# Optimization experiments

Measured on AMD Instinct MI355X. Metric: run time of the kernel, lower is better.

The kernel has to match this reference:

```python
import jax, jax.numpy as jnp
import numpy as np

N = 50000      # nodes
E = 800000     # edges (avg degree 16)
IN = 128       # in_dim == hidden_dim*num_heads so residuals fire
D = 32         # hidden_dim (per-head)
H = 4          # num_heads
OUT = 64       # out_dim (final layer has 1 head)
NEG_SLOPE = 0.2
LN_EPS = 1e-5


def setup_inputs() -> dict:
    key = jax.random.key(0)
    ks = jax.random.split(key, 16)
    rn = lambda k, s: jax.random.normal(k, s, jnp.float32) * 0.05
    return {
        "features": jax.random.normal(ks[0], (N, IN), jnp.float32),
        "edge_weight": jax.random.uniform(ks[1], (E,), jnp.float32),
        "src": jax.random.randint(ks[2], (E,), 0, N),
        "dst": jax.random.randint(ks[3], (E,), 0, N),
        "W0": rn(ks[4], (IN, H * D)), "al0": rn(ks[5], (H, D)), "ar0": rn(ks[6], (H, D)), "lam0": jnp.float32(1.0),
        "W1": rn(ks[7], (H * D, H * D)), "al1": rn(ks[8], (H, D)), "ar1": rn(ks[9], (H, D)), "lam1": jnp.float32(1.0),
        "W2": rn(ks[10], (H * D, OUT)), "al2": rn(ks[11], (1, OUT)), "ar2": rn(ks[12], (1, OUT)), "lam2": jnp.float32(1.0),
        "g0": jnp.ones((H * D,), jnp.float32), "b0": jnp.zeros((H * D,), jnp.float32),
        "g1": jnp.ones((H * D,), jnp.float32), "b1": jnp.zeros((H * D,), jnp.float32),
    }


def _gat_layer(h, W, al, ar, lam, src, dst, ew):
    n = h.shape[0]
    heads, d = al.shape
    ft = (h @ W).reshape(n, heads, d)                      # [N,H,D]
    el = jnp.sum(ft * al[None], axis=-1)                   # [N,H]
    er = jnp.sum(ft * ar[None], axis=-1)                   # [N,H]
    e = el[src] + er[dst] + lam * ew[:, None]              # [E,H] u_add_v + weight bias
    e = jax.nn.leaky_relu(e, NEG_SLOPE)
    # edge softmax over incoming edges of each dst node
    m = jax.ops.segment_max(e, dst, num_segments=n)        # [N,H]
    ex = jnp.exp(e - m[dst])
    s = jax.ops.segment_sum(ex, dst, num_segments=n)       # [N,H]
    a = ex / s[dst]                                        # [E,H]
    # u_mul_e + sum aggregation
    msg = ft[src] * a[:, :, None]                          # [E,H,D]
    return jax.ops.segment_sum(msg, dst, num_segments=n)   # [N,H,D]


def _layer_norm(x, g, b):
    mu = jnp.mean(x, axis=-1, keepdims=True)
    var = jnp.mean((x - mu) ** 2, axis=-1, keepdims=True)
    return (x - mu) * jax.lax.rsqrt(var + LN_EPS) * g + b


def _forward(features, edge_weight, src, dst,
             W0, al0, ar0, lam0, W1, al1, ar1, lam1, W2, al2, ar2, lam2,
             g0, b0, g1, b1):
    n = features.shape[0]
    h = features
    # layer 0
    h1 = _gat_layer(h, W0, al0, ar0, lam0, src, dst, edge_weight)
    h1 = jax.nn.elu(h1).reshape(n, -1)
    h1 = _layer_norm(h1, g0, b0)
    if h1.shape == h.shape:
        h1 = h1 + h
    # layer 1
    h2 = _gat_layer(h1, W1, al1, ar1, lam1, src, dst, edge_weight)
    h2 = jax.nn.elu(h2).reshape(n, -1)
    h2 = _layer_norm(h2, g1, b1)
    h2 = h2 + h1
    # layer 2 (single head, no activation)
    out = _gat_layer(h2, W2, al2, ar2, lam2, src, dst, edge_weight).reshape(n, -1)
    return out


def reference(features, edge_weight, src, dst,
              W0, al0, ar0, lam0, W1, al1, ar1, lam1, W2, al2, ar2, lam2,
              g0, b0, g1, b1):
    # eval mode: dropout off and _add_noise is identity, so noisy == clean
    h_clean = _forward(features, edge_weight, src, dst,
                       W0, al0, ar0, lam0, W1, al1, ar1, lam1, W2, al2, ar2, lam2,
                       g0, b0, g1, b1)
    return (h_clean, h_clean)
```

## Files before the change

kernel.cpp:

```cpp
#include <hip/hip_runtime.h>

#define NEG_SLOPE 0.2f
#define LN_EPS 1e-5f

typedef __attribute__((ext_vector_type(8))) short bf16x8;
typedef __attribute__((ext_vector_type(4))) float f32x4;

__device__ inline unsigned short f2bf(float f) {
    unsigned u = __float_as_uint(f);
    unsigned r = u + 0x7FFFu + ((u >> 16) & 1u);
    return (unsigned short)(r >> 16);
}

__device__ inline void unpack8(uint4 u, float* f) {
    f[0] = __uint_as_float(u.x << 16);
    f[1] = __uint_as_float(u.x & 0xFFFF0000u);
    f[2] = __uint_as_float(u.y << 16);
    f[3] = __uint_as_float(u.y & 0xFFFF0000u);
    f[4] = __uint_as_float(u.z << 16);
    f[5] = __uint_as_float(u.z & 0xFFFF0000u);
    f[6] = __uint_as_float(u.w << 16);
    f[7] = __uint_as_float(u.w & 0xFFFF0000u);
}


__global__ void prep_kernel(const int* __restrict__ dst, int* __restrict__ counts,
                            int* __restrict__ rank, int E, int RB,
                            const float* __restrict__ W0, const float* __restrict__ W1,
                            const float* __restrict__ W2, unsigned short* __restrict__ Wt0,
                            unsigned short* __restrict__ Wt1,
                            unsigned short* __restrict__ Wt2) {
    int bid = blockIdx.x;
    if (bid < RB) {
        int i = bid * 256 + threadIdx.x;
        if (i < E) rank[i] = atomicAdd(&counts[dst[i] * 16], 1);
    } else {
        int row = (bid - RB) * 2 + (threadIdx.x >> 7);
        int k = threadIdx.x & 127;
        if (row < 128) {
            Wt0[row * 128 + k] = f2bf(W0[k * 128 + row]);
        } else if (row < 256) {
            int c = row - 128;
            Wt1[c * 128 + k] = f2bf(W1[k * 128 + c]);
        } else {
            int c = row - 256;
            Wt2[c * 128 + k] = f2bf(W2[k * 64 + c]);
        }
    }
}

__global__ __launch_bounds__(256) void scan1_kernel(const int* __restrict__ counts,
                                                    int* __restrict__ bsum, int n) {
    __shared__ int lds[256];
    int t = threadIdx.x;
    int i = blockIdx.x * 256 + t;
    lds[t] = (i < n) ? counts[i * 16] : 0;
    __syncthreads();
    for (int off = 128; off > 0; off >>= 1) {
        int v = (t < off) ? lds[t + off] : 0;
        __syncthreads();
        if (t < off) lds[t] += v;
        __syncthreads();
    }
    if (t == 0) bsum[blockIdx.x] = lds[0];
}

__global__ __launch_bounds__(256) void scan3_kernel(const int* __restrict__ counts,
                                                    const int* __restrict__ bsum,
                                                    int* __restrict__ rowptr, int n, int E,
                                                    int nscan) {
    __shared__ int lds[256];
    int t = threadIdx.x;
    lds[t] = (t < nscan) ? bsum[t] : 0;
    __syncthreads();
    for (int off = 1; off < 256; off <<= 1) {
        int v = (t >= off) ? lds[t - off] : 0;
        __syncthreads();
        lds[t] += v;
        __syncthreads();
    }
    int boff = (blockIdx.x > 0) ? lds[blockIdx.x - 1] : 0;
    __syncthreads();
    int i = blockIdx.x * 256 + t;
    int c = (i < n) ? counts[i * 16] : 0;
    lds[t] = c;
    __syncthreads();
    for (int off = 1; off < 256; off <<= 1) {
        int v = (t >= off) ? lds[t - off] : 0;
        __syncthreads();
        lds[t] += v;
        __syncthreads();
    }
    if (i < n) rowptr[i] = boff + lds[t] - c;
    if (i == n) rowptr[n] = E;
}

__global__ void place_kernel(const int* __restrict__ src, const int* __restrict__ dst,
                             const float* __restrict__ ew, const int* __restrict__ rowptr,
                             const int* __restrict__ rank, unsigned* __restrict__ edge_p,
                             int E) {
    int i = blockIdx.x * blockDim.x + threadIdx.x;
    if (i < E) {
        int p = rowptr[dst[i]] + rank[i];
        edge_p[p] = ((unsigned)f2bf(ew[i]) << 16) | (unsigned)src[i];
    }
}


template <int NT, int H, bool A32>
__global__ __launch_bounds__(256) void gemm_mfma(const void* __restrict__ Ap,
                                                 const unsigned short* __restrict__ Wt,
                                                 const float* __restrict__ al,
                                                 const float* __restrict__ ar,
                                                 unsigned short* __restrict__ ftb,
                                                 float* __restrict__ el,
                                                 float* __restrict__ er, int n) {
    constexpr int LDA = 136;
    constexpr int D = NT * 16 / H;
    __shared__ unsigned short As[64 * LDA];
    __shared__ unsigned short Ws[NT * 16 * LDA];
    int t = threadIdx.x;
    int row0 = blockIdx.x * 64;

    if constexpr (A32) {
        const float4* A4 = (const float4*)Ap;
        #pragma unroll
        for (int j = 0; j < 8; ++j) {
            int idx = t + j * 256;
            int r = idx >> 5;
            int c4 = idx & 31;
            int row = row0 + r;
            float4 v = (row < n) ? A4[(size_t)row * 32 + c4] : make_float4(0.f, 0.f, 0.f, 0.f);
            unsigned p0 = (unsigned)f2bf(v.x) | ((unsigned)f2bf(v.y) << 16);
            unsigned p1 = (unsigned)f2bf(v.z) | ((unsigned)f2bf(v.w) << 16);
            *(uint2*)&As[r * LDA + c4 * 4] = make_uint2(p0, p1);
        }
    } else {
        const uint4* A16 = (const uint4*)Ap;
        #pragma unroll
        for (int j = 0; j < 4; ++j) {
            int idx = t + j * 256;
            int r = idx >> 4;
            int c8 = idx & 15;
            int row = row0 + r;
            uint4 v = (row < n) ? A16[(size_t)row * 16 + c8] : make_uint4(0, 0, 0, 0);
            *(uint4*)&As[r * LDA + c8 * 8] = v;
        }
    }
    const uint4* Wg = (const uint4*)Wt;
    #pragma unroll
    for (int j = 0; j < NT; ++j) {
        int idx = t + j * 256;
        int r = idx >> 4;
        int c8 = idx & 15;
        *(uint4*)&Ws[r * LDA + c8 * 8] = Wg[idx];
    }
    __syncthreads();

    int w = t >> 6, lane = t & 63;
    int m = lane & 15, q = lane >> 4;
    f32x4 acc[NT] = {};
    const unsigned short* ap = &As[(w * 16 + m) * LDA + q * 8];
    #pragma unroll
    for (int kk = 0; kk < 4; ++kk) {
        bf16x8 a = *(const bf16x8*)(ap + kk * 32);
        #pragma unroll
        for (int nt = 0; nt < NT; ++nt) {
            bf16x8 b = *(const bf16x8*)&Ws[(nt * 16 + m) * LDA + kk * 32 + q * 8];
            acc[nt] = __builtin_amdgcn_mfma_f32_16x16x32_bf16(a, b, acc[nt], 0, 0, 0);
        }
    }

    float alv[NT], arv[NT];
    #pragma unroll
    for (int nt = 0; nt < NT; ++nt) {
        alv[nt] = al[nt * 16 + m];
        arv[nt] = ar[nt * 16 + m];
    }

    int orow = row0 + w * 16 + q * 4;
    #pragma unroll
    for (int r = 0; r < 4; ++r) {
        int row = orow + r;
        float pl[H] = {}, pr[H] = {};
        #pragma unroll
        for (int nt = 0; nt < NT; ++nt) {
            int h = (nt * 16) / D;
            pl[h] = fmaf(acc[nt][r], alv[nt], pl[h]);
            pr[h] = fmaf(acc[nt][r], arv[nt], pr[h]);
        }
        #pragma unroll
        for (int off = 1; off < 16; off <<= 1) {
            #pragma unroll
            for (int h = 0; h < H; ++h) {
                pl[h] += __shfl_xor(pl[h], off, 64);
                pr[h] += __shfl_xor(pr[h], off, 64);
            }
        }
        if (row < n) {
            #pragma unroll
            for (int nt = 0; nt < NT; ++nt)
                ftb[(size_t)row * (NT * 16) + nt * 16 + m] = f2bf(acc[nt][r]);
            if (m < H) {
                float vl = pl[0], vr = pr[0];
                #pragma unroll
                for (int h = 1; h < H; ++h)
                    if (m == h) { vl = pl[h]; vr = pr[h]; }
                el[row * H + m] = vl;
                er[row * H + m] = vr;
            }
        }
    }
}


__device__ inline void accum8(float* ax, uint4 u, float p) {
    ax[0] = fmaf(p, __uint_as_float(u.x << 16), ax[0]);
    ax[1] = fmaf(p, __uint_as_float(u.x & 0xFFFF0000u), ax[1]);
    ax[2] = fmaf(p, __uint_as_float(u.y << 16), ax[2]);
    ax[3] = fmaf(p, __uint_as_float(u.y & 0xFFFF0000u), ax[3]);
    ax[4] = fmaf(p, __uint_as_float(u.z << 16), ax[4]);
    ax[5] = fmaf(p, __uint_as_float(u.z & 0xFFFF0000u), ax[5]);
    ax[6] = fmaf(p, __uint_as_float(u.w << 16), ax[6]);
    ax[7] = fmaf(p, __uint_as_float(u.w & 0xFFFF0000u), ax[7]);
}

template <bool PREV32>
__global__ __launch_bounds__(256) void gat_agg_ln(
    const int* __restrict__ rowptr, const unsigned* __restrict__ edge_p,
    const uint4* __restrict__ ftb4, const float* __restrict__ el,
    const float* __restrict__ er, const float* __restrict__ lam_p,
    const float* __restrict__ g, const float* __restrict__ b,
    const void* __restrict__ prevp, uint4* __restrict__ outb, int n) {
    int node = blockIdx.x * 16 + (threadIdx.x >> 4);
    if (node >= n) return;
    int li = threadIdx.x & 15;
    int head = li >> 2;
    float lam = lam_p[0];
    float erv = er[node * 4 + head];
    int s0 = rowptr[node], s1 = rowptr[node + 1];
    float ax[8] = {};
    float s = 0.f;

    int i = s0;
    for (; i + 4 <= s1; i += 4) {
        unsigned e0 = edge_p[i], e1 = edge_p[i + 1], e2 = edge_p[i + 2], e3 = edge_p[i + 3];
        unsigned sn0 = e0 & 0xFFFFu, sn1 = e1 & 0xFFFFu, sn2 = e2 & 0xFFFFu, sn3 = e3 & 0xFFFFu;
        uint4 u0 = ftb4[(size_t)sn0 * 16 + li];
        uint4 u1 = ftb4[(size_t)sn1 * 16 + li];
        uint4 u2 = ftb4[(size_t)sn2 * 16 + li];
        uint4 u3 = ftb4[(size_t)sn3 * 16 + li];
        float l0 = el[sn0 * 4 + head];
        float l1 = el[sn1 * 4 + head];
        float l2 = el[sn2 * 4 + head];
        float l3 = el[sn3 * 4 + head];
        float v0 = l0 + erv + lam * __uint_as_float(e0 & 0xFFFF0000u);
        float v1 = l1 + erv + lam * __uint_as_float(e1 & 0xFFFF0000u);
        float v2 = l2 + erv + lam * __uint_as_float(e2 & 0xFFFF0000u);
        float v3 = l3 + erv + lam * __uint_as_float(e3 & 0xFFFF0000u);
        v0 = fmaxf(v0, NEG_SLOPE * v0);
        v1 = fmaxf(v1, NEG_SLOPE * v1);
        v2 = fmaxf(v2, NEG_SLOPE * v2);
        v3 = fmaxf(v3, NEG_SLOPE * v3);
        float p0 = __expf(v0), p1 = __expf(v1), p2 = __expf(v2), p3 = __expf(v3);
        accum8(ax, u0, p0);
        accum8(ax, u1, p1);
        accum8(ax, u2, p2);
        accum8(ax, u3, p3);
        s += (p0 + p1) + (p2 + p3);
    }
    for (; i < s1; ++i) {
        unsigned e = edge_p[i];
        unsigned sn = e & 0xFFFFu;
        uint4 u = ftb4[(size_t)sn * 16 + li];
        float v = el[sn * 4 + head] + erv + lam * __uint_as_float(e & 0xFFFF0000u);
        v = fmaxf(v, NEG_SLOPE * v);
        float p = __expf(v);
        accum8(ax, u, p);
        s += p;
    }

    float inv = (s > 0.f) ? 1.f / s : 0.f;
    float x[8];
    float sum = 0.f, sq = 0.f;
    #pragma unroll
    for (int d = 0; d < 8; ++d) {
        float v = ax[d] * inv;
        v = (v > 0.f) ? v : expm1f(v);
        x[d] = v;
        sum += v;
        sq += v * v;
    }
    #pragma unroll
    for (int off = 1; off < 16; off <<= 1) {
        sum += __shfl_xor(sum, off, 16);
        sq += __shfl_xor(sq, off, 16);
    }
    float mu = sum * (1.f / 128.f);
    float var = sq * (1.f / 128.f) - mu * mu;
    float rs = rsqrtf(var + LN_EPS);

    const float4* g4 = (const float4*)g;
    const float4* b4 = (const float4*)b;
    float pv[8];
    if constexpr (PREV32) {
        const float4* p4 = (const float4*)prevp;
        #pragma unroll
        for (int h = 0; h < 2; ++h) {
            float4 v = p4[(size_t)node * 32 + li * 2 + h];
            pv[h * 4 + 0] = v.x; pv[h * 4 + 1] = v.y;
            pv[h * 4 + 2] = v.z; pv[h * 4 + 3] = v.w;
        }
    } else {
        unpack8(((const uint4*)prevp)[(size_t)node * 16 + li], pv);
    }
    float y[8];
    #pragma unroll
    for (int h = 0; h < 2; ++h) {
        float4 gv = g4[li * 2 + h];
        float4 bv = b4[li * 2 + h];
        y[h * 4 + 0] = (x[h * 4 + 0] - mu) * rs * gv.x + bv.x + pv[h * 4 + 0];
        y[h * 4 + 1] = (x[h * 4 + 1] - mu) * rs * gv.y + bv.y + pv[h * 4 + 1];
        y[h * 4 + 2] = (x[h * 4 + 2] - mu) * rs * gv.z + bv.z + pv[h * 4 + 2];
        y[h * 4 + 3] = (x[h * 4 + 3] - mu) * rs * gv.w + bv.w + pv[h * 4 + 3];
    }
    uint4 o;
    o.x = (unsigned)f2bf(y[0]) | ((unsigned)f2bf(y[1]) << 16);
    o.y = (unsigned)f2bf(y[2]) | ((unsigned)f2bf(y[3]) << 16);
    o.z = (unsigned)f2bf(y[4]) | ((unsigned)f2bf(y[5]) << 16);
    o.w = (unsigned)f2bf(y[6]) | ((unsigned)f2bf(y[7]) << 16);
    outb[(size_t)node * 16 + li] = o;
}

__global__ __launch_bounds__(256) void gat_agg_out(
    const int* __restrict__ rowptr, const unsigned* __restrict__ edge_p,
    const uint2* __restrict__ ftb2, const float* __restrict__ el,
    const float* __restrict__ er, const float* __restrict__ lam_p,
    float* __restrict__ out, int n) {
    int node = blockIdx.x * 16 + (threadIdx.x >> 4);
    if (node >= n) return;
    int li = threadIdx.x & 15;
    float lam = lam_p[0];
    float erv = er[node];
    int s0 = rowptr[node], s1 = rowptr[node + 1];
    float ax[4] = {};
    float s = 0.f;

    int i = s0;
    for (; i + 4 <= s1; i += 4) {
        unsigned e0 = edge_p[i], e1 = edge_p[i + 1], e2 = edge_p[i + 2], e3 = edge_p[i + 3];
        unsigned sn0 = e0 & 0xFFFFu, sn1 = e1 & 0xFFFFu, sn2 = e2 & 0xFFFFu, sn3 = e3 & 0xFFFFu;
        uint2 u0 = ftb2[(size_t)sn0 * 16 + li];
        uint2 u1 = ftb2[(size_t)sn1 * 16 + li];
        uint2 u2 = ftb2[(size_t)sn2 * 16 + li];
        uint2 u3 = ftb2[(size_t)sn3 * 16 + li];
        float l0 = el[sn0], l1 = el[sn1], l2 = el[sn2], l3 = el[sn3];
        float v0 = l0 + erv + lam * __uint_as_float(e0 & 0xFFFF0000u);
        float v1 = l1 + erv + lam * __uint_as_float(e1 & 0xFFFF0000u);
        float v2 = l2 + erv + lam * __uint_as_float(e2 & 0xFFFF0000u);
        float v3 = l3 + erv + lam * __uint_as_float(e3 & 0xFFFF0000u);
        v0 = fmaxf(v0, NEG_SLOPE * v0);
        v1 = fmaxf(v1, NEG_SLOPE * v1);
        v2 = fmaxf(v2, NEG_SLOPE * v2);
        v3 = fmaxf(v3, NEG_SLOPE * v3);
        float p0 = __expf(v0), p1 = __expf(v1), p2 = __expf(v2), p3 = __expf(v3);
        ax[0] = fmaf(p0, __uint_as_float(u0.x << 16), ax[0]);
        ax[1] = fmaf(p0, __uint_as_float(u0.x & 0xFFFF0000u), ax[1]);
        ax[2] = fmaf(p0, __uint_as_float(u0.y << 16), ax[2]);
        ax[3] = fmaf(p0, __uint_as_float(u0.y & 0xFFFF0000u), ax[3]);
        ax[0] = fmaf(p1, __uint_as_float(u1.x << 16), ax[0]);
        ax[1] = fmaf(p1, __uint_as_float(u1.x & 0xFFFF0000u), ax[1]);
        ax[2] = fmaf(p1, __uint_as_float(u1.y << 16), ax[2]);
        ax[3] = fmaf(p1, __uint_as_float(u1.y & 0xFFFF0000u), ax[3]);
        ax[0] = fmaf(p2, __uint_as_float(u2.x << 16), ax[0]);
        ax[1] = fmaf(p2, __uint_as_float(u2.x & 0xFFFF0000u), ax[1]);
        ax[2] = fmaf(p2, __uint_as_float(u2.y << 16), ax[2]);
        ax[3] = fmaf(p2, __uint_as_float(u2.y & 0xFFFF0000u), ax[3]);
        ax[0] = fmaf(p3, __uint_as_float(u3.x << 16), ax[0]);
        ax[1] = fmaf(p3, __uint_as_float(u3.x & 0xFFFF0000u), ax[1]);
        ax[2] = fmaf(p3, __uint_as_float(u3.y << 16), ax[2]);
        ax[3] = fmaf(p3, __uint_as_float(u3.y & 0xFFFF0000u), ax[3]);
        s += (p0 + p1) + (p2 + p3);
    }
    for (; i < s1; ++i) {
        unsigned e = edge_p[i];
        unsigned sn = e & 0xFFFFu;
        uint2 u = ftb2[(size_t)sn * 16 + li];
        float v = el[sn] + erv + lam * __uint_as_float(e & 0xFFFF0000u);
        v = fmaxf(v, NEG_SLOPE * v);
        float p = __expf(v);
        ax[0] = fmaf(p, __uint_as_float(u.x << 16), ax[0]);
        ax[1] = fmaf(p, __uint_as_float(u.x & 0xFFFF0000u), ax[1]);
        ax[2] = fmaf(p, __uint_as_float(u.y << 16), ax[2]);
        ax[3] = fmaf(p, __uint_as_float(u.y & 0xFFFF0000u), ax[3]);
        s += p;
    }

    float inv = (s > 0.f) ? 1.f / s : 0.f;
    float4 y;
    y.x = ax[0] * inv;
    y.y = ax[1] * inv;
    y.z = ax[2] * inv;
    y.w = ax[3] * inv;
    ((float4*)out)[(size_t)node * 16 + li] = y;
    ((float4*)out)[(size_t)(n + node) * 16 + li] = y;
}


extern "C" void kernel_launch(void* const* d_in, const int* in_sizes, int n_in,
                              void* d_out, int out_size, void* d_ws, size_t ws_size,
                              hipStream_t stream) {
    const float* features = (const float*)d_in[0];
    const float* edge_weight = (const float*)d_in[1];
    const int* src = (const int*)d_in[2];
    const int* dst = (const int*)d_in[3];
    const float* W0 = (const float*)d_in[4];
    const float* al0 = (const float*)d_in[5];
    const float* ar0 = (const float*)d_in[6];
    const float* lam0 = (const float*)d_in[7];
    const float* W1 = (const float*)d_in[8];
    const float* al1 = (const float*)d_in[9];
    const float* ar1 = (const float*)d_in[10];
    const float* lam1 = (const float*)d_in[11];
    const float* W2 = (const float*)d_in[12];
    const float* al2 = (const float*)d_in[13];
    const float* ar2 = (const float*)d_in[14];
    const float* lam2 = (const float*)d_in[15];
    const float* g0 = (const float*)d_in[16];
    const float* b0 = (const float*)d_in[17];
    const float* g1 = (const float*)d_in[18];
    const float* b1 = (const float*)d_in[19];

    const int N = in_sizes[0] / 128;
    const int E = in_sizes[1];

    char* w = (char*)d_ws;
    size_t o = 0;
    auto carve = [&](size_t bytes) {
        char* p = w + o;
        o += (bytes + 255) & ~(size_t)255;
        return p;
    };
    int* counts = (int*)carve((size_t)N * 64);
    int* rowptr = (int*)carve((size_t)(N + 1) * 4);
    int* bsum = (int*)carve(256 * 4);
    int* rank = (int*)carve((size_t)E * 4);
    unsigned* edge_p = (unsigned*)carve((size_t)E * 4);
    unsigned short* ftb = (unsigned short*)carve((size_t)N * 128 * 2);
    unsigned short* h1 = (unsigned short*)carve((size_t)N * 128 * 2);
    unsigned short* h2 = (unsigned short*)carve((size_t)N * 128 * 2);
    float* el = (float*)carve((size_t)N * 4 * 4);
    float* er = (float*)carve((size_t)N * 4 * 4);
    unsigned short* Wt0 = (unsigned short*)carve(128 * 128 * 2);
    unsigned short* Wt1 = (unsigned short*)carve(128 * 128 * 2);
    unsigned short* Wt2 = (unsigned short*)carve(64 * 128 * 2);

    const int nscan = (N + 255) / 256;
    const int ngemm = (N + 63) / 64;
    const int nagg = (N + 15) / 16;
    const int RB = (E + 255) / 256;

    hipMemsetAsync(counts, 0, (size_t)N * 64, stream);
    prep_kernel<<<RB + 160, 256, 0, stream>>>(dst, counts, rank, E, RB,
                                              W0, W1, W2, Wt0, Wt1, Wt2);
    scan1_kernel<<<nscan, 256, 0, stream>>>(counts, bsum, N);
    scan3_kernel<<<(N + 1 + 255) / 256, 256, 0, stream>>>(counts, bsum, rowptr, N, E, nscan);
    place_kernel<<<(E + 255) / 256, 256, 0, stream>>>(src, dst, edge_weight, rowptr,
                                                      rank, edge_p, E);

    gemm_mfma<8, 4, true><<<ngemm, 256, 0, stream>>>(features, Wt0, al0, ar0,
                                                     ftb, el, er, N);
    gat_agg_ln<true><<<nagg, 256, 0, stream>>>(rowptr, edge_p, (const uint4*)ftb, el, er,
                                               lam0, g0, b0, features, (uint4*)h1, N);
    gemm_mfma<8, 4, false><<<ngemm, 256, 0, stream>>>(h1, Wt1, al1, ar1, ftb, el, er, N);
    gat_agg_ln<false><<<nagg, 256, 0, stream>>>(rowptr, edge_p, (const uint4*)ftb, el, er,
                                                lam1, g1, b1, h1, (uint4*)h2, N);
    gemm_mfma<4, 1, false><<<ngemm, 256, 0, stream>>>(h2, Wt2, al2, ar2, ftb, el, er, N);
    gat_agg_out<<<nagg, 256, 0, stream>>>(rowptr, edge_p, (const uint2*)ftb,
                                          el, er, lam2, (float*)d_out, N);
}
```

Baseline: 296.6 us.

## Degree-sort nodes for aggregation and batch edge gathers via lane shuffles

Builds a degree histogram during the scan and a counting-sort permutation of nodes by descending in-degree in the place kernel, so aggregation wavefronts process nodes of similar degree together and divergence is reduced. Edge records are now loaded cooperatively, one per lane in chunks of 16, and broadcast with shuffles, with up to 8 feature gathers issued per batch to raise memory-level parallelism. In exchange, node outputs and er reads become scattered through the permutation, and a small extra sorting pass is added.

```diff
diff --git a/kernel.cpp b/kernel.cpp
--- a/kernel.cpp
+++ b/kernel.cpp
@@ -50,12 +50,17 @@
 }
 
 __global__ __launch_bounds__(256) void scan1_kernel(const int* __restrict__ counts,
-                                                    int* __restrict__ bsum, int n) {
+                                                    int* __restrict__ bsum,
+                                                    int* __restrict__ dhist, int n) {
     __shared__ int lds[256];
+    __shared__ int hbin[64];
     int t = threadIdx.x;
+    if (t < 64) hbin[t] = 0;
     int i = blockIdx.x * 256 + t;
-    lds[t] = (i < n) ? counts[i * 16] : 0;
+    int c = (i < n) ? counts[i * 16] : 0;
+    lds[t] = c;
     __syncthreads();
+    if (i < n) atomicAdd(&hbin[63 - (c < 63 ? c : 63)], 1);
     for (int off = 128; off > 0; off >>= 1) {
         int v = (t < off) ? lds[t + off] : 0;
         __syncthreads();
@@ -63,12 +68,18 @@
         __syncthreads();
     }
     if (t == 0) bsum[blockIdx.x] = lds[0];
+    if (t < 64) {
+        int h = hbin[t];
+        if (h) atomicAdd(&dhist[t], h);
+    }
 }
 
 __global__ __launch_bounds__(256) void scan3_kernel(const int* __restrict__ counts,
                                                     const int* __restrict__ bsum,
-                                                    int* __restrict__ rowptr, int n, int E,
-                                                    int nscan) {
+                                                    int* __restrict__ rowptr,
+                                                    const int* __restrict__ dhist,
+                                                    int* __restrict__ dbase,
+                                                    int n, int E, int nscan) {
     __shared__ int lds[256];
     int t = threadIdx.x;
     lds[t] = (t < nscan) ? bsum[t] : 0;
@@ -93,16 +104,49 @@
     }
     if (i < n) rowptr[i] = boff + lds[t] - c;
     if (i == n) rowptr[n] = E;
-}
-
-__global__ void place_kernel(const int* __restrict__ src, const int* __restrict__ dst,
-                             const float* __restrict__ ew, const int* __restrict__ rowptr,
-                             const int* __restrict__ rank, unsigned* __restrict__ edge_p,
-                             int E) {
-    int i = blockIdx.x * blockDim.x + threadIdx.x;
-    if (i < E) {
-        int p = rowptr[dst[i]] + rank[i];
-        edge_p[p] = ((unsigned)f2bf(ew[i]) << 16) | (unsigned)src[i];
+    if (blockIdx.x == 0 && t < 64) {
+        int v = dhist[t];
+        int x = v;
+        #pragma unroll
+        for (int off = 1; off < 64; off <<= 1) {
+            int u = __shfl_up(x, off, 64);
+            if (t >= off) x += u;
+        }
+        dbase[t] = x - v;
+    }
+}
+
+__global__ __launch_bounds__(256) void place_kernel(
+    const int* __restrict__ src, const int* __restrict__ dst,
+    const float* __restrict__ ew, const int* __restrict__ rowptr,
+    const int* __restrict__ rank, unsigned* __restrict__ edge_p,
+    const int* __restrict__ dbase, int* __restrict__ dcount,
+    int* __restrict__ perm, int E, int EB, int N) {
+    __shared__ int lbin[64];
+    __shared__ int lbase[64];
+    int bid = blockIdx.x;
+    int t = threadIdx.x;
+    if (bid < EB) {
+        int i = bid * 256 + t;
+        if (i < E) {
+            int p = rowptr[dst[i]] + rank[i];
+            edge_p[p] = ((unsigned)f2bf(ew[i]) << 16) | (unsigned)src[i];
+        }
+    } else {
+        if (t < 64) lbin[t] = 0;
+        __syncthreads();
+        int nidx = (bid - EB) * 256 + t;
+        bool valid = nidx < N;
+        int key = 0, myoff = 0;
+        if (valid) {
+            int deg = rowptr[nidx + 1] - rowptr[nidx];
+            key = 63 - (deg < 63 ? deg : 63);
+            myoff = atomicAdd(&lbin[key], 1);
+        }
+        __syncthreads();
+        if (t < 64) lbase[t] = lbin[t] ? atomicAdd(&dcount[t], lbin[t]) : 0;
+        __syncthreads();
+        if (valid) perm[dbase[key] + lbase[key] + myoff] = nidx;
     }
 }
 
@@ -225,15 +269,76 @@
     ax[7] = fmaf(p, __uint_as_float(u.w & 0xFFFF0000u), ax[7]);
 }
 
+__device__ inline void accum4(float* ax, uint2 u, float p) {
+    ax[0] = fmaf(p, __uint_as_float(u.x << 16), ax[0]);
+    ax[1] = fmaf(p, __uint_as_float(u.x & 0xFFFF0000u), ax[1]);
+    ax[2] = fmaf(p, __uint_as_float(u.y << 16), ax[2]);
+    ax[3] = fmaf(p, __uint_as_float(u.y & 0xFFFF0000u), ax[3]);
+}
+
+template <int K>
+__device__ inline void agg_batch(const uint4* __restrict__ ftb4,
+                                 const float* __restrict__ el, unsigned ev, int j,
+                                 int li, int head, float erv, float lam, float* ax,
+                                 float& s) {
+    unsigned ee[K];
+    uint4 uu[K];
+    float ll[K];
+    #pragma unroll
+    for (int k = 0; k < K; ++k) ee[k] = __shfl(ev, j + k, 16);
+    #pragma unroll
+    for (int k = 0; k < K; ++k) {
+        unsigned sn = ee[k] & 0xFFFFu;
+        uu[k] = ftb4[(size_t)sn * 16 + li];
+        ll[k] = el[sn * 4 + head];
+    }
+    #pragma unroll
+    for (int k = 0; k < K; ++k) {
+        float v = ll[k] + erv + lam * __uint_as_float(ee[k] & 0xFFFF0000u);
+        v = fmaxf(v, NEG_SLOPE * v);
+        float p = __expf(v);
+        accum8(ax, uu[k], p);
+        s += p;
+    }
+}
+
+template <int K>
+__device__ inline void agg_batch_out(const uint2* __restrict__ ftb2,
+                                     const float* __restrict__ el, unsigned ev,
+                                     int j, int li, float erv, float lam, float* ax,
+                                     float& s) {
+    unsigned ee[K];
+    uint2 uu[K];
+    float ll[K];
+    #pragma unroll
+    for (int k = 0; k < K; ++k) ee[k] = __shfl(ev, j + k, 16);
+    #pragma unroll
+    for (int k = 0; k < K; ++k) {
+        unsigned sn = ee[k] & 0xFFFFu;
+        uu[k] = ftb2[(size_t)sn * 16 + li];
+        ll[k] = el[sn];
+    }
+    #pragma unroll
+    for (int k = 0; k < K; ++k) {
+        float v = ll[k] + erv + lam * __uint_as_float(ee[k] & 0xFFFF0000u);
+        v = fmaxf(v, NEG_SLOPE * v);
+        float p = __expf(v);
+        accum4(ax, uu[k], p);
+        s += p;
+    }
+}
+
 template <bool PREV32>
 __global__ __launch_bounds__(256) void gat_agg_ln(
     const int* __restrict__ rowptr, const unsigned* __restrict__ edge_p,
-    const uint4* __restrict__ ftb4, const float* __restrict__ el,
-    const float* __restrict__ er, const float* __restrict__ lam_p,
-    const float* __restrict__ g, const float* __restrict__ b,
-    const void* __restrict__ prevp, uint4* __restrict__ outb, int n) {
-    int node = blockIdx.x * 16 + (threadIdx.x >> 4);
-    if (node >= n) return;
+    const int* __restrict__ perm, const uint4* __restrict__ ftb4,
+    const float* __restrict__ el, const float* __restrict__ er,
+    const float* __restrict__ lam_p, const float* __restrict__ g,
+    const float* __restrict__ b, const void* __restrict__ prevp,
+    uint4* __restrict__ outb, int n) {
+    int gid = blockIdx.x * 16 + (threadIdx.x >> 4);
+    if (gid >= n) return;
+    int node = perm[gid];
     int li = threadIdx.x & 15;
     int head = li >> 2;
     float lam = lam_p[0];
@@ -242,42 +347,19 @@
     float ax[8] = {};
     float s = 0.f;
 
-    int i = s0;
-    for (; i + 4 <= s1; i += 4) {
-        unsigned e0 = edge_p[i], e1 = edge_p[i + 1], e2 = edge_p[i + 2], e3 = edge_p[i + 3];
-        unsigned sn0 = e0 & 0xFFFFu, sn1 = e1 & 0xFFFFu, sn2 = e2 & 0xFFFFu, sn3 = e3 & 0xFFFFu;
-        uint4 u0 = ftb4[(size_t)sn0 * 16 + li];
-        uint4 u1 = ftb4[(size_t)sn1 * 16 + li];
-        uint4 u2 = ftb4[(size_t)sn2 * 16 + li];
-        uint4 u3 = ftb4[(size_t)sn3 * 16 + li];
-        float l0 = el[sn0 * 4 + head];
-        float l1 = el[sn1 * 4 + head];
-        float l2 = el[sn2 * 4 + head];
-        float l3 = el[sn3 * 4 + head];
-        float v0 = l0 + erv + lam * __uint_as_float(e0 & 0xFFFF0000u);
-        float v1 = l1 + erv + lam * __uint_as_float(e1 & 0xFFFF0000u);
-        float v2 = l2 + erv + lam * __uint_as_float(e2 & 0xFFFF0000u);
-        float v3 = l3 + erv + lam * __uint_as_float(e3 & 0xFFFF0000u);
-        v0 = fmaxf(v0, NEG_SLOPE * v0);
-        v1 = fmaxf(v1, NEG_SLOPE * v1);
-        v2 = fmaxf(v2, NEG_SLOPE * v2);
-        v3 = fmaxf(v3, NEG_SLOPE * v3);
-        float p0 = __expf(v0), p1 = __expf(v1), p2 = __expf(v2), p3 = __expf(v3);
-        accum8(ax, u0, p0);
-        accum8(ax, u1, p1);
-        accum8(ax, u2, p2);
-        accum8(ax, u3, p3);
-        s += (p0 + p1) + (p2 + p3);
-    }
-    for (; i < s1; ++i) {
-        unsigned e = edge_p[i];
-        unsigned sn = e & 0xFFFFu;
-        uint4 u = ftb4[(size_t)sn * 16 + li];
-        float v = el[sn * 4 + head] + erv + lam * __uint_as_float(e & 0xFFFF0000u);
-        v = fmaxf(v, NEG_SLOPE * v);
-        float p = __expf(v);
-        accum8(ax, u, p);
-        s += p;
+    for (int base = s0; base < s1; base += 16) {
+        int m = s1 - base;
+        if (m > 16) m = 16;
+        unsigned ev = (li < m) ? edge_p[base + li] : 0u;
+        int j = 0;
+        for (; j + 8 <= m; j += 8)
+            agg_batch<8>(ftb4, el, ev, j, li, head, erv, lam, ax, s);
+        if (j + 4 <= m) {
+            agg_batch<4>(ftb4, el, ev, j, li, head, erv, lam, ax, s);
+            j += 4;
+        }
+        for (; j < m; ++j)
+            agg_batch<1>(ftb4, el, ev, j, li, head, erv, lam, ax, s);
     }
 
     float inv = (s > 0.f) ? 1.f / s : 0.f;
@@ -334,11 +416,12 @@
 
 __global__ __launch_bounds__(256) void gat_agg_out(
     const int* __restrict__ rowptr, const unsigned* __restrict__ edge_p,
-    const uint2* __restrict__ ftb2, const float* __restrict__ el,
-    const float* __restrict__ er, const float* __restrict__ lam_p,
-    float* __restrict__ out, int n) {
-    int node = blockIdx.x * 16 + (threadIdx.x >> 4);
-    if (node >= n) return;
+    const int* __restrict__ perm, const uint2* __restrict__ ftb2,
+    const float* __restrict__ el, const float* __restrict__ er,
+    const float* __restrict__ lam_p, float* __restrict__ out, int n) {
+    int gid = blockIdx.x * 16 + (threadIdx.x >> 4);
+    if (gid >= n) return;
+    int node = perm[gid];
     int li = threadIdx.x & 15;
     float lam = lam_p[0];
     float erv = er[node];
@@ -346,54 +429,19 @@
     float ax[4] = {};
     float s = 0.f;
 
-    int i = s0;
-    for (; i + 4 <= s1; i += 4) {
-        unsigned e0 = edge_p[i], e1 = edge_p[i + 1], e2 = edge_p[i + 2], e3 = edge_p[i + 3];
-        unsigned sn0 = e0 & 0xFFFFu, sn1 = e1 & 0xFFFFu, sn2 = e2 & 0xFFFFu, sn3 = e3 & 0xFFFFu;
-        uint2 u0 = ftb2[(size_t)sn0 * 16 + li];
-        uint2 u1 = ftb2[(size_t)sn1 * 16 + li];
-        uint2 u2 = ftb2[(size_t)sn2 * 16 + li];
-        uint2 u3 = ftb2[(size_t)sn3 * 16 + li];
-        float l0 = el[sn0], l1 = el[sn1], l2 = el[sn2], l3 = el[sn3];
-        float v0 = l0 + erv + lam * __uint_as_float(e0 & 0xFFFF0000u);
-        float v1 = l1 + erv + lam * __uint_as_float(e1 & 0xFFFF0000u);
-        float v2 = l2 + erv + lam * __uint_as_float(e2 & 0xFFFF0000u);
-        float v3 = l3 + erv + lam * __uint_as_float(e3 & 0xFFFF0000u);
-        v0 = fmaxf(v0, NEG_SLOPE * v0);
-        v1 = fmaxf(v1, NEG_SLOPE * v1);
-        v2 = fmaxf(v2, NEG_SLOPE * v2);
-        v3 = fmaxf(v3, NEG_SLOPE * v3);
-        float p0 = __expf(v0), p1 = __expf(v1), p2 = __expf(v2), p3 = __expf(v3);
-        ax[0] = fmaf(p0, __uint_as_float(u0.x << 16), ax[0]);
-        ax[1] = fmaf(p0, __uint_as_float(u0.x & 0xFFFF0000u), ax[1]);
-        ax[2] = fmaf(p0, __uint_as_float(u0.y << 16), ax[2]);
-        ax[3] = fmaf(p0, __uint_as_float(u0.y & 0xFFFF0000u), ax[3]);
-        ax[0] = fmaf(p1, __uint_as_float(u1.x << 16), ax[0]);
-        ax[1] = fmaf(p1, __uint_as_float(u1.x & 0xFFFF0000u), ax[1]);
-        ax[2] = fmaf(p1, __uint_as_float(u1.y << 16), ax[2]);
-        ax[3] = fmaf(p1, __uint_as_float(u1.y & 0xFFFF0000u), ax[3]);
-        ax[0] = fmaf(p2, __uint_as_float(u2.x << 16), ax[0]);
-        ax[1] = fmaf(p2, __uint_as_float(u2.x & 0xFFFF0000u), ax[1]);
-        ax[2] = fmaf(p2, __uint_as_float(u2.y << 16), ax[2]);
-        ax[3] = fmaf(p2, __uint_as_float(u2.y & 0xFFFF0000u), ax[3]);
-        ax[0] = fmaf(p3, __uint_as_float(u3.x << 16), ax[0]);
-        ax[1] = fmaf(p3, __uint_as_float(u3.x & 0xFFFF0000u), ax[1]);
-        ax[2] = fmaf(p3, __uint_as_float(u3.y << 16), ax[2]);
-        ax[3] = fmaf(p3, __uint_as_float(u3.y & 0xFFFF0000u), ax[3]);
-        s += (p0 + p1) + (p2 + p3);
-    }
-    for (; i < s1; ++i) {
-        unsigned e = edge_p[i];
-        unsigned sn = e & 0xFFFFu;
-        uint2 u = ftb2[(size_t)sn * 16 + li];
-        float v = el[sn] + erv + lam * __uint_as_float(e & 0xFFFF0000u);
-        v = fmaxf(v, NEG_SLOPE * v);
-        float p = __expf(v);
-        ax[0] = fmaf(p, __uint_as_float(u.x << 16), ax[0]);
-        ax[1] = fmaf(p, __uint_as_float(u.x & 0xFFFF0000u), ax[1]);
-        ax[2] = fmaf(p, __uint_as_float(u.y << 16), ax[2]);
-        ax[3] = fmaf(p, __uint_as_float(u.y & 0xFFFF0000u), ax[3]);
-        s += p;
+    for (int base = s0; base < s1; base += 16) {
+        int m = s1 - base;
+        if (m > 16) m = 16;
+        unsigned ev = (li < m) ? edge_p[base + li] : 0u;
+        int j = 0;
+        for (; j + 8 <= m; j += 8)
+            agg_batch_out<8>(ftb2, el, ev, j, li, erv, lam, ax, s);
+        if (j + 4 <= m) {
+            agg_batch_out<4>(ftb2, el, ev, j, li, erv, lam, ax, s);
+            j += 4;
+        }
+        for (; j < m; ++j)
+            agg_batch_out<1>(ftb2, el, ev, j, li, erv, lam, ax, s);
     }
 
     float inv = (s > 0.f) ? 1.f / s : 0.f;
@@ -442,10 +490,14 @@
         return p;
     };
     int* counts = (int*)carve((size_t)N * 64);
+    int* dhist = (int*)carve(256);
+    int* dcount = (int*)carve(256);
     int* rowptr = (int*)carve((size_t)(N + 1) * 4);
     int* bsum = (int*)carve(256 * 4);
     int* rank = (int*)carve((size_t)E * 4);
     unsigned* edge_p = (unsigned*)carve((size_t)E * 4);
+    int* dbase = (int*)carve(256);
+    int* perm = (int*)carve((size_t)N * 4);
     unsigned short* ftb = (unsigned short*)carve((size_t)N * 128 * 2);
     unsigned short* h1 = (unsigned short*)carve((size_t)N * 128 * 2);
     unsigned short* h2 = (unsigned short*)carve((size_t)N * 128 * 2);
@@ -460,22 +512,24 @@
     const int nagg = (N + 15) / 16;
     const int RB = (E + 255) / 256;
 
-    hipMemsetAsync(counts, 0, (size_t)N * 64, stream);
+    hipMemsetAsync(counts, 0, (size_t)N * 64 + 512, stream);
     prep_kernel<<<RB + 160, 256, 0, stream>>>(dst, counts, rank, E, RB,
                                               W0, W1, W2, Wt0, Wt1, Wt2);
-    scan1_kernel<<<nscan, 256, 0, stream>>>(counts, bsum, N);
-    scan3_kernel<<<(N + 1 + 255) / 256, 256, 0, stream>>>(counts, bsum, rowptr, N, E, nscan);
-    place_kernel<<<(E + 255) / 256, 256, 0, stream>>>(src, dst, edge_weight, rowptr,
-                                                      rank, edge_p, E);
+    scan1_kernel<<<nscan, 256, 0, stream>>>(counts, bsum, dhist, N);
+    scan3_kernel<<<(N + 1 + 255) / 256, 256, 0, stream>>>(counts, bsum, rowptr,
+                                                          dhist, dbase, N, E, nscan);
+    place_kernel<<<RB + nscan, 256, 0, stream>>>(src, dst, edge_weight, rowptr, rank,
+                                                 edge_p, dbase, dcount, perm, E, RB, N);
 
     gemm_mfma<8, 4, true><<<ngemm, 256, 0, stream>>>(features, Wt0, al0, ar0,
                                                      ftb, el, er, N);
-    gat_agg_ln<true><<<nagg, 256, 0, stream>>>(rowptr, edge_p, (const uint4*)ftb, el, er,
-                                               lam0, g0, b0, features, (uint4*)h1, N);
+    gat_agg_ln<true><<<nagg, 256, 0, stream>>>(rowptr, edge_p, perm, (const uint4*)ftb,
+                                               el, er, lam0, g0, b0, features,
+                                               (uint4*)h1, N);
     gemm_mfma<8, 4, false><<<ngemm, 256, 0, stream>>>(h1, Wt1, al1, ar1, ftb, el, er, N);
-    gat_agg_ln<false><<<nagg, 256, 0, stream>>>(rowptr, edge_p, (const uint4*)ftb, el, er,
-                                                lam1, g1, b1, h1, (uint4*)h2, N);
+    gat_agg_ln<false><<<nagg, 256, 0, stream>>>(rowptr, edge_p, perm, (const uint4*)ftb,
+                                                el, er, lam1, g1, b1, h1, (uint4*)h2, N);
     gemm_mfma<4, 1, false><<<ngemm, 256, 0, stream>>>(h2, Wt2, al2, ar2, ftb, el, er, N);
-    gat_agg_out<<<nagg, 256, 0, stream>>>(rowptr, edge_p, (const uint2*)ftb,
+    gat_agg_out<<<nagg, 256, 0, stream>>>(rowptr, edge_p, perm, (const uint2*)ftb,
                                           el, er, lam2, (float*)d_out, N);
 }
```

Measured after the change: 294.5 us. Within noise of the previous version (-0.7%).
